# Kernel tuning notes

Measured on AMD Instinct MI355X. Metric: run time of the kernel, lower is better.

## Reference

```python
import jax, jax.numpy as jnp
import numpy as np

B, C_IN, C_OUT, H, W = 8, 64, 64, 128, 128
G, K, PAD = 8, 3, 1
CG_OUT = C_OUT // G   # 8
CG_IN = C_IN // G     # 8


def setup_inputs() -> dict:
    key = jax.random.key(0)
    ks = jax.random.split(key, 6)
    x = jax.random.normal(ks[0], (B, C_IN, H, W), dtype=jnp.float32)
    # grouped 1x1 conv weights, stored as (groups, out_per_group, in_per_group)
    scale = (2.0 / C_OUT) ** 0.5  # kaiming fan_out
    Wq = jax.random.normal(ks[1], (G, CG_OUT, CG_IN), dtype=jnp.float32) * scale
    Wk = jax.random.normal(ks[2], (G, CG_OUT, CG_IN), dtype=jnp.float32) * scale
    Wv = jax.random.normal(ks[3], (G, CG_OUT, CG_IN), dtype=jnp.float32) * scale
    h_emb = jax.random.normal(ks[4], (G, CG_OUT // 2, 1, 1, K, 1), dtype=jnp.float32)
    w_emb = jax.random.normal(ks[5], (G, CG_OUT // 2, 1, 1, 1, K), dtype=jnp.float32)
    return {"x": x, "Wq": Wq, "Wk": Wk, "Wv": Wv, "h_emb": h_emb, "w_emb": w_emb}


def _gconv1x1(x, Wt):
    # grouped 1x1 conv: x (B,C,H,W) -> (B,G,Cg,H,W)
    b, c, h, w = x.shape
    xg = x.reshape(b, G, c // G, h, w)
    return jnp.einsum('bgihw,goi->bgohw', xg, Wt)


def _unfold(t):
    # t: (B,G,Cg,H+2p,W+2p) -> (B,G,Cg,H,W,K*K), window index = i*K + j (h-major,
    # matching torch unfold(2).unfold(3).view)
    slices = [t[..., i:i + H, j:j + W] for i in range(K) for j in range(K)]
    return jnp.stack(slices, axis=-1)


def reference(x, Wq, Wk, Wv, h_emb, w_emb):
    x_pad = jnp.pad(x, ((0, 0), (0, 0), (PAD, PAD), (PAD, PAD)))
    q = _gconv1x1(x, Wq)            # (B,G,Cg,H,W)
    kf = _gconv1x1(x_pad, Wk)       # (B,G,Cg,H+2,W+2)
    vf = _gconv1x1(x_pad, Wv)
    kp = _unfold(kf)                # (B,G,Cg,H,W,K^2)
    vp = _unfold(vf)
    # relative position embedding: h half broadcast over w, w half over h
    he = jnp.broadcast_to(h_emb, (G, CG_OUT // 2, 1, 1, K, K))
    we = jnp.broadcast_to(w_emb, (G, CG_OUT // 2, 1, 1, K, K))
    emb = jnp.concatenate([he, we], axis=1).reshape(G, CG_OUT, 1, 1, K * K)
    logits = q[..., None] * (kp + emb[None])       # (B,G,Cg,H,W,K^2)
    attn = jax.nn.softmax(logits, axis=-1)
    out = jnp.sum(attn * vp, axis=-1)              # (B,G,Cg,H,W)
    return out.reshape(x.shape[0], C_OUT, H, W)
```

## Files before the change

kernel.cpp:

```cpp
#include <hip/hip_runtime.h>


#define HH 128
#define WW 128
#define HW (HH * WW)
#define TS 32
#define PT 34
#define PTP 35
#define LOG2E 1.44269504088896f

__global__ __launch_bounds__(256) void sab_fused(
    const float* __restrict__ x,
    const float* __restrict__ Wq,
    const float* __restrict__ Wk,
    const float* __restrict__ Wv,
    const float* __restrict__ h_emb,
    const float* __restrict__ w_emb,
    float* __restrict__ out)
{
    __shared__ float2 kv[4][PT][PTP];
    __shared__ float wk_s[64], wv_s[64], wq_s[64], emb_s[72];

    const int bid0 = blockIdx.x;
    const int bid  = (bid0 & 7) * 128 + (bid0 >> 3);

    const int tile = bid & 15;
    const int bg   = bid >> 4;
    const int g    = bg & 7;
    const int b    = bg >> 3;
    const int h0   = (tile >> 2) << 5;
    const int w0   = (tile & 3) << 5;
    const int tid  = threadIdx.x;
    const int tx   = tid & 31;
    const int ty   = tid >> 5;
    const int r0   = ty << 2;

    if (tid < 64) {
        wk_s[tid] = Wk[g * 64 + tid];
        wv_s[tid] = Wv[g * 64 + tid];
        wq_s[tid] = Wq[g * 64 + tid];
    } else if (tid < 64 + 72) {
        int t = tid - 64;
        int c = t / 9, p = t % 9;
        int ki = p / 3, kj = p % 3;
        emb_s[t] = (c < 4) ? h_emb[(g * 4 + c) * 3 + ki]
                           : w_emb[(g * 4 + (c - 4)) * 3 + kj];
    }

    const float* xb = x + ((size_t)(b * 64 + g * 8)) * HW;

    float xi[4][8];
    #pragma unroll
    for (int r = 0; r < 4; r++) {
        const int base = (h0 + r0 + r) * WW + (w0 + tx);
        #pragma unroll
        for (int i = 0; i < 8; i++)
            xi[r][i] = xb[i * HW + base];
    }

    float hx[8];
    int hpy = 0, hpx = 0;
    const bool is_halo = tid < 132;
    if (is_halo) {
        if (tid < 34)       { hpy = 0;         hpx = tid; }
        else if (tid < 68)  { hpy = 33;        hpx = tid - 34; }
        else if (tid < 100) { hpy = tid - 67;  hpx = 0; }
        else                { hpy = tid - 99;  hpx = 33; }
        const int gh = h0 + hpy - 1, gw = w0 + hpx - 1;
        const bool ok = (gh >= 0) & (gh < HH) & (gw >= 0) & (gw < WW);
        const int base = gh * WW + gw;
        #pragma unroll
        for (int i = 0; i < 8; i++)
            hx[i] = ok ? xb[i * HW + base] : 0.0f;
    }

    __syncthreads();

    float* const ob = out + ((size_t)(b * 64 + g * 8)) * HW;

    #pragma unroll
    for (int c0 = 0; c0 < 8; c0 += 4) {
        if (c0 != 0) __syncthreads();

        float q[4][4];
        #pragma unroll
        for (int cc = 0; cc < 4; cc++) {
            const int c = c0 + cc;
            float wkr[8], wvr[8], wqr[8];
            #pragma unroll
            for (int i = 0; i < 8; i++) {
                wkr[i] = wk_s[c * 8 + i];
                wvr[i] = wv_s[c * 8 + i];
                wqr[i] = wq_s[c * 8 + i];
            }
            #pragma unroll
            for (int r = 0; r < 4; r++) {
                float kk = 0.0f, vv = 0.0f, qq = 0.0f;
                #pragma unroll
                for (int i = 0; i < 8; i++) {
                    kk = fmaf(wkr[i], xi[r][i], kk);
                    vv = fmaf(wvr[i], xi[r][i], vv);
                    qq = fmaf(wqr[i], xi[r][i], qq);
                }
                kv[cc][r0 + 1 + r][tx + 1] = make_float2(kk, vv);
                q[cc][r] = qq * LOG2E;
            }
            if (is_halo) {
                float kk = 0.0f, vv = 0.0f;
                #pragma unroll
                for (int i = 0; i < 8; i++) {
                    kk = fmaf(wkr[i], hx[i], kk);
                    vv = fmaf(wvr[i], hx[i], vv);
                }
                kv[cc][hpy][hpx] = make_float2(kk, vv);
            }
        }
        __syncthreads();

        #pragma unroll
        for (int cc = 0; cc < 4; cc++) {
            const int c = c0 + cc;
            float eb[9];
            #pragma unroll
            for (int p = 0; p < 9; p++) eb[p] = emb_s[c * 9 + p];

            float2 win[6][3];
            #pragma unroll
            for (int rr = 0; rr < 6; rr++)
                #pragma unroll
                for (int jj = 0; jj < 3; jj++)
                    win[rr][jj] = kv[cc][r0 + rr][tx + jj];

            float* oc = ob + (size_t)c * HW + (h0 + r0) * WW + (w0 + tx);
            #pragma unroll
            for (int r = 0; r < 4; r++) {
                const float ql = q[cc][r];
                float s = 0.0f, o = 0.0f;
                #pragma unroll
                for (int p = 0; p < 9; p++) {
                    const float2 t = win[r + p / 3][p % 3];
                    const float e = __builtin_amdgcn_exp2f(ql * (t.x + eb[p]));
                    s += e;
                    o = fmaf(e, t.y, o);
                }
                oc[r * WW] = o * __builtin_amdgcn_rcpf(s);
            }
        }
    }
}

extern "C" void kernel_launch(void* const* d_in, const int* in_sizes, int n_in,
                              void* d_out, int out_size, void* d_ws, size_t ws_size,
                              hipStream_t stream) {
    const float* x    = (const float*)d_in[0];
    const float* Wq   = (const float*)d_in[1];
    const float* Wk   = (const float*)d_in[2];
    const float* Wv   = (const float*)d_in[3];
    const float* h_e  = (const float*)d_in[4];
    const float* w_e  = (const float*)d_in[5];
    float* out = (float*)d_out;

    dim3 grid(8 * 8 * 16);
    dim3 block(256);
    sab_fused<<<grid, block, 0, stream>>>(x, Wq, Wk, Wv, h_e, w_e, out);
}
```

Baseline: 32.02 us.

## Split output channels across blocks and vectorize loads/stores with float4

Each block now handles only 2 of the 8 output channels of a group tile, giving four times as many blocks. Each thread covers 4 adjacent pixels in one row, so input loads and output stores use float4. Weights and embeddings are read straight into registers instead of shared memory, and shared memory shrinks so more blocks can be resident (launch bounds request 5). The cost is that every block re-reads the same 8 input channels and halo, so input traffic and the 1x1 conv for K/V are repeated four times per tile.

Result: faster. 29.07 us (-9.2%).

```diff
diff --git a/kernel.cpp b/kernel.cpp
--- a/kernel.cpp
+++ b/kernel.cpp
@@ -4,12 +4,11 @@
 #define HH 128
 #define WW 128
 #define HW (HH * WW)
-#define TS 32
 #define PT 34
 #define PTP 35
 #define LOG2E 1.44269504088896f
 
-__global__ __launch_bounds__(256) void sab_fused(
+__global__ __launch_bounds__(256, 5) void sab_fused(
     const float* __restrict__ x,
     const float* __restrict__ Wq,
     const float* __restrict__ Wk,
@@ -18,134 +17,120 @@
     const float* __restrict__ w_emb,
     float* __restrict__ out)
 {
-    __shared__ float2 kv[4][PT][PTP];
-    __shared__ float wk_s[64], wv_s[64], wq_s[64], emb_s[72];
+    __shared__ float2 kv[2][PT][PTP];
 
     const int bid0 = blockIdx.x;
-    const int bid  = (bid0 & 7) * 128 + (bid0 >> 3);
-
-    const int tile = bid & 15;
-    const int bg   = bid >> 4;
+    const int work = (bid0 & 7) * 512 + (bid0 >> 3);
+    const int c0   = (work & 3) << 1;
+    const int tile = (work >> 2) & 15;
+    const int bg   = work >> 6;
     const int g    = bg & 7;
     const int b    = bg >> 3;
     const int h0   = (tile >> 2) << 5;
     const int w0   = (tile & 3) << 5;
     const int tid  = threadIdx.x;
-    const int tx   = tid & 31;
-    const int ty   = tid >> 5;
-    const int r0   = ty << 2;
+    const int ty   = tid >> 3;
+    const int x0   = (tid & 7) << 2;
 
-    if (tid < 64) {
-        wk_s[tid] = Wk[g * 64 + tid];
-        wv_s[tid] = Wv[g * 64 + tid];
-        wq_s[tid] = Wq[g * 64 + tid];
-    } else if (tid < 64 + 72) {
-        int t = tid - 64;
-        int c = t / 9, p = t % 9;
-        int ki = p / 3, kj = p % 3;
-        emb_s[t] = (c < 4) ? h_emb[(g * 4 + c) * 3 + ki]
-                           : w_emb[(g * 4 + (c - 4)) * 3 + kj];
+    float wk[2][8], wv[2][8], wq[2][8], eb[2][9];
+    #pragma unroll
+    for (int cc = 0; cc < 2; cc++) {
+        const int c = c0 + cc;
+        #pragma unroll
+        for (int i = 0; i < 8; i++) {
+            wk[cc][i] = Wk[g * 64 + c * 8 + i];
+            wv[cc][i] = Wv[g * 64 + c * 8 + i];
+            wq[cc][i] = Wq[g * 64 + c * 8 + i];
+        }
+        #pragma unroll
+        for (int p = 0; p < 9; p++) {
+            eb[cc][p] = (c < 4) ? h_emb[(g * 4 + c) * 3 + p / 3]
+                                : w_emb[(g * 4 + c - 4) * 3 + p % 3];
+        }
     }
 
-    const float* xb = x + ((size_t)(b * 64 + g * 8)) * HW;
+    const float* xb = x + (size_t)(b * 64 + g * 8) * HW;
+    const int ibase = (h0 + ty) * WW + (w0 + x0);
 
-    float xi[4][8];
+    float4 xi[8];
     #pragma unroll
-    for (int r = 0; r < 4; r++) {
-        const int base = (h0 + r0 + r) * WW + (w0 + tx);
+    for (int i = 0; i < 8; i++)
+        xi[i] = *reinterpret_cast<const float4*>(xb + i * HW + ibase);
+
+    float kk[2][4], vv[2][4], qq[2][4];
+    #pragma unroll
+    for (int cc = 0; cc < 2; cc++)
         #pragma unroll
-        for (int i = 0; i < 8; i++)
-            xi[r][i] = xb[i * HW + base];
+        for (int px = 0; px < 4; px++) { kk[cc][px] = 0.f; vv[cc][px] = 0.f; qq[cc][px] = 0.f; }
+
+    #pragma unroll
+    for (int i = 0; i < 8; i++) {
+        const float4 xv = xi[i];
+        const float xs[4] = {xv.x, xv.y, xv.z, xv.w};
+        #pragma unroll
+        for (int cc = 0; cc < 2; cc++)
+            #pragma unroll
+            for (int px = 0; px < 4; px++) {
+                kk[cc][px] = fmaf(wk[cc][i], xs[px], kk[cc][px]);
+                vv[cc][px] = fmaf(wv[cc][i], xs[px], vv[cc][px]);
+                qq[cc][px] = fmaf(wq[cc][i], xs[px], qq[cc][px]);
+            }
     }
+    #pragma unroll
+    for (int cc = 0; cc < 2; cc++)
+        #pragma unroll
+        for (int px = 0; px < 4; px++)
+            kv[cc][ty + 1][x0 + 1 + px] = make_float2(kk[cc][px], vv[cc][px]);
 
-    float hx[8];
-    int hpy = 0, hpx = 0;
-    const bool is_halo = tid < 132;
-    if (is_halo) {
-        if (tid < 34)       { hpy = 0;         hpx = tid; }
-        else if (tid < 68)  { hpy = 33;        hpx = tid - 34; }
-        else if (tid < 100) { hpy = tid - 67;  hpx = 0; }
-        else                { hpy = tid - 99;  hpx = 33; }
+    if (tid < 132) {
+        int hpy, hpx;
+        if (tid < 34)       { hpy = 0;        hpx = tid; }
+        else if (tid < 68)  { hpy = 33;       hpx = tid - 34; }
+        else if (tid < 100) { hpy = tid - 67; hpx = 0; }
+        else                { hpy = tid - 99; hpx = 33; }
         const int gh = h0 + hpy - 1, gw = w0 + hpx - 1;
         const bool ok = (gh >= 0) & (gh < HH) & (gw >= 0) & (gw < WW);
         const int base = gh * WW + gw;
+        float hk[2] = {0.f, 0.f}, hv[2] = {0.f, 0.f};
         #pragma unroll
-        for (int i = 0; i < 8; i++)
-            hx[i] = ok ? xb[i * HW + base] : 0.0f;
+        for (int i = 0; i < 8; i++) {
+            const float xv = ok ? xb[i * HW + base] : 0.0f;
+            hk[0] = fmaf(wk[0][i], xv, hk[0]);
+            hv[0] = fmaf(wv[0][i], xv, hv[0]);
+            hk[1] = fmaf(wk[1][i], xv, hk[1]);
+            hv[1] = fmaf(wv[1][i], xv, hv[1]);
+        }
+        kv[0][hpy][hpx] = make_float2(hk[0], hv[0]);
+        kv[1][hpy][hpx] = make_float2(hk[1], hv[1]);
     }
 
     __syncthreads();
 
-    float* const ob = out + ((size_t)(b * 64 + g * 8)) * HW;
+    #pragma unroll
+    for (int cc = 0; cc < 2; cc++) {
+        float2 win[3][6];
+        #pragma unroll
+        for (int r = 0; r < 3; r++)
+            #pragma unroll
+            for (int j = 0; j < 6; j++)
+                win[r][j] = kv[cc][ty + r][x0 + j];
 
-    #pragma unroll
-    for (int c0 = 0; c0 < 8; c0 += 4) {
-        if (c0 != 0) __syncthreads();
-
-        float q[4][4];
+        float o4[4];
         #pragma unroll
-        for (int cc = 0; cc < 4; cc++) {
-            const int c = c0 + cc;
-            float wkr[8], wvr[8], wqr[8];
+        for (int px = 0; px < 4; px++) {
+            const float ql = qq[cc][px] * LOG2E;
+            float s = 0.0f, o = 0.0f;
             #pragma unroll
-            for (int i = 0; i < 8; i++) {
-                wkr[i] = wk_s[c * 8 + i];
-                wvr[i] = wv_s[c * 8 + i];
-                wqr[i] = wq_s[c * 8 + i];
+            for (int p = 0; p < 9; p++) {
+                const float2 t = win[p / 3][px + p % 3];
+                const float e = __builtin_amdgcn_exp2f(ql * (t.x + eb[cc][p]));
+                s += e;
+                o = fmaf(e, t.y, o);
             }
-            #pragma unroll
-            for (int r = 0; r < 4; r++) {
-                float kk = 0.0f, vv = 0.0f, qq = 0.0f;
-                #pragma unroll
-                for (int i = 0; i < 8; i++) {
-                    kk = fmaf(wkr[i], xi[r][i], kk);
-                    vv = fmaf(wvr[i], xi[r][i], vv);
-                    qq = fmaf(wqr[i], xi[r][i], qq);
-                }
-                kv[cc][r0 + 1 + r][tx + 1] = make_float2(kk, vv);
-                q[cc][r] = qq * LOG2E;
-            }
-            if (is_halo) {
-                float kk = 0.0f, vv = 0.0f;
-                #pragma unroll
-                for (int i = 0; i < 8; i++) {
-                    kk = fmaf(wkr[i], hx[i], kk);
-                    vv = fmaf(wvr[i], hx[i], vv);
-                }
-                kv[cc][hpy][hpx] = make_float2(kk, vv);
-            }
+            o4[px] = o * __builtin_amdgcn_rcpf(s);
         }
-        __syncthreads();
-
-        #pragma unroll
-        for (int cc = 0; cc < 4; cc++) {
-            const int c = c0 + cc;
-            float eb[9];
-            #pragma unroll
-            for (int p = 0; p < 9; p++) eb[p] = emb_s[c * 9 + p];
-
-            float2 win[6][3];
-            #pragma unroll
-            for (int rr = 0; rr < 6; rr++)
-                #pragma unroll
-                for (int jj = 0; jj < 3; jj++)
-                    win[rr][jj] = kv[cc][r0 + rr][tx + jj];
-
-            float* oc = ob + (size_t)c * HW + (h0 + r0) * WW + (w0 + tx);
-            #pragma unroll
-            for (int r = 0; r < 4; r++) {
-                const float ql = q[cc][r];
-                float s = 0.0f, o = 0.0f;
-                #pragma unroll
-                for (int p = 0; p < 9; p++) {
-                    const float2 t = win[r + p / 3][p % 3];
-                    const float e = __builtin_amdgcn_exp2f(ql * (t.x + eb[p]));
-                    s += e;
-                    o = fmaf(e, t.y, o);
-                }
-                oc[r * WW] = o * __builtin_amdgcn_rcpf(s);
-            }
-        }
+        *reinterpret_cast<float4*>(out + (size_t)(b * 64 + g * 8 + c0 + cc) * HW + ibase)
+            = make_float4(o4[0], o4[1], o4[2], o4[3]);
     }
 }
 
@@ -160,7 +145,7 @@
     const float* w_e  = (const float*)d_in[5];
     float* out = (float*)d_out;
 
-    dim3 grid(8 * 8 * 16);
+    dim3 grid(8 * 8 * 16 * 4);
     dim3 block(256);
     sab_fused<<<grid, block, 0, stream>>>(x, Wq, Wk, Wv, h_e, w_e, out);
 }
```
